# Kernel tuning notes

Measured on AMD Instinct MI355X. Metric: run time of the kernel, lower is better.

The kernel has to match this reference:

```python
import jax, jax.numpy as jnp
import numpy as np

B, S, D, H, DH = 2, 4096, 768, 12, 64
L = 2                      # encoder layers (reduced-depth longformer-base)
HW = 256                   # one-sided sliding window (attention_window = 512)
C = 2 * HW                 # query chunk size
NC = S // C                # number of chunks
KW = C + 2 * HW            # key-window length per chunk
V = 50265
SEP_ID, NSEP = 2, 32       # </s> token id; SEPs per block (fixed by construction)
G = NSEP + 1               # global tokens: <s> at pos 0 + all SEPs
NCLS = 5
EPS = 1e-5
NEG = -1e9


def layer_norm(x, gb):
    m = jnp.mean(x, -1, keepdims=True)
    v = jnp.var(x, -1, keepdims=True)
    return (x - m) * jax.lax.rsqrt(v + EPS) * gb[0] + gb[1]


def split_heads(x):  # [B,S,D] -> [B,H,S,DH]
    return x.reshape(B, S, H, DH).transpose(0, 2, 1, 3)


def window_gather(x):  # [B,H,S,DH] -> [B,H,NC,KW,DH] overlapping key windows
    xp = jnp.pad(x, ((0, 0), (0, 0), (HW, HW), (0, 0)))
    idx = (jnp.arange(NC) * C)[:, None] + jnp.arange(KW)[None, :]
    return xp[:, :, idx, :]


def longformer_attn(x, amask, gpos, wqkv, bqkv, wqkv_g, bqkv_g, wo, bo):
    q = split_heads(x @ wqkv[0] + bqkv[0]) / np.float32(np.sqrt(DH))
    k = split_heads(x @ wqkv[1] + bqkv[1])
    v = split_heads(x @ wqkv[2] + bqkv[2])

    # ----- local sliding-window scores (banded, chunked) -----
    kw = window_gather(k)
    vw = window_gather(v)
    qc = q.reshape(B, H, NC, C, DH)
    s_loc = jnp.einsum('bhncd,bhnkd->bhnck', qc, kw)  # [B,H,NC,C,KW]

    rel = jnp.arange(KW)[None, :] - jnp.arange(C)[:, None]          # [C,KW]
    band_ok = (rel >= 0) & (rel <= 2 * HW)
    key_pos = (jnp.arange(NC) * C)[:, None] + jnp.arange(KW)[None, :] - HW
    in_b = (key_pos >= 0) & (key_pos < S)                            # [NC,KW]
    amp = jnp.pad(amask, ((0, 0), (HW, HW)))
    idx = (jnp.arange(NC) * C)[:, None] + jnp.arange(KW)[None, :]
    am_w = amp[:, idx] > 0                                           # [B,NC,KW]
    mask = band_ok[None, None, None] & in_b[None, None, :, None, :] & am_w[:, None, :, None, :]
    s_loc = jnp.where(mask, s_loc, NEG).reshape(B, H, S, KW)

    # ----- scores of every query against the G global keys -----
    gidx = gpos[:, None, :, None]                                    # [B,1,G,1]
    kg = jnp.take_along_axis(k, gidx, axis=2)                        # [B,H,G,DH]
    vg = jnp.take_along_axis(v, gidx, axis=2)
    s_glob = jnp.einsum('bhsd,bhgd->bhsg', q, kg)                    # [B,H,S,G]

    probs = jax.nn.softmax(jnp.concatenate([s_glob, s_loc], -1), -1)
    pg, pl = probs[..., :G], probs[..., G:]
    ctx = jnp.einsum('bhsg,bhgd->bhsd', pg, vg)
    ctx = ctx + jnp.einsum('bhnck,bhnkd->bhncd', pl.reshape(B, H, NC, C, KW), vw).reshape(B, H, S, DH)

    # ----- global tokens attend to everything (separate projections) -----
    qg = split_heads(x @ wqkv_g[0] + bqkv_g[0]) / np.float32(np.sqrt(DH))
    kgf = split_heads(x @ wqkv_g[1] + bqkv_g[1])
    vgf = split_heads(x @ wqkv_g[2] + bqkv_g[2])
    qg = jnp.take_along_axis(qg, gidx, axis=2)                       # [B,H,G,DH]
    s_g = jnp.einsum('bhgd,bhsd->bhgs', qg, kgf)                     # [B,H,G,S]
    s_g = jnp.where(amask[:, None, None, :] > 0, s_g, NEG)
    og = jnp.einsum('bhgs,bhsd->bhgd', jax.nn.softmax(s_g, -1), vgf)

    ctx_m = ctx.transpose(0, 2, 1, 3).reshape(B, S, D)
    og_m = og.transpose(0, 2, 1, 3).reshape(B, G, D)
    ctx_m = ctx_m.at[jnp.arange(B)[:, None], gpos].set(og_m)         # replace global rows
    return ctx_m @ wo + bo


def setup_inputs() -> dict:
    key = jax.random.key(0)
    ks = jax.random.split(key, 12)
    ids = jax.random.randint(ks[0], (B, S), 5, V, dtype=jnp.int32)
    sep_positions = (jnp.arange(NSEP) + 1) * (S // NSEP) - 1         # SEP every 128 toks
    ids = ids.at[:, sep_positions].set(SEP_ID).at[:, 0].set(0)       # <s> at pos 0
    att = jnp.ones((B, S), jnp.int32)

    def nrm(k, shp):
        return jax.random.normal(k, shp, jnp.float32) * 0.02

    ln = jnp.stack([jnp.ones(D, jnp.float32), jnp.zeros(D, jnp.float32)])
    return dict(
        input_ids=ids, attention_mask=att,
        word_emb=nrm(ks[1], (V, D)), pos_emb=nrm(ks[2], (S + 2, D)),
        type_emb=nrm(ks[3], (D,)), emb_ln=ln,
        Wqkv=nrm(ks[4], (L, 3, D, D)), bqkv=jnp.zeros((L, 3, D), jnp.float32),
        Wqkv_g=nrm(ks[5], (L, 3, D, D)), bqkv_g=jnp.zeros((L, 3, D), jnp.float32),
        Wo=nrm(ks[6], (L, D, D)), bo=jnp.zeros((L, D), jnp.float32),
        ln1=jnp.broadcast_to(ln, (L, 2, D)),
        Wff1=nrm(ks[7], (L, D, 4 * D)), bff1=jnp.zeros((L, 4 * D), jnp.float32),
        Wff2=nrm(ks[8], (L, 4 * D, D)), bff2=jnp.zeros((L, D), jnp.float32),
        ln2=jnp.broadcast_to(ln, (L, 2, D)),
        cls_W=nrm(ks[9], (NCLS, D)), cls_b=jnp.zeros((NCLS,), jnp.float32),
    )


def reference(input_ids, attention_mask, word_emb, pos_emb, type_emb, emb_ln,
              Wqkv, bqkv, Wqkv_g, bqkv_g, Wo, bo, ln1, Wff1, bff1, Wff2, bff2,
              ln2, cls_W, cls_b):
    # global attention mask: pos 0 + every SEP (fixed count by construction)
    sep_pos = jnp.sort(jnp.where(input_ids == SEP_ID, jnp.arange(S)[None, :], S), -1)[:, :NSEP]
    sep_pos = sep_pos.astype(jnp.int32)
    gpos = jnp.concatenate([jnp.zeros((B, 1), jnp.int32), sep_pos], 1)  # [B,G]

    x = word_emb[input_ids] + pos_emb[jnp.arange(S) + 2][None] + type_emb
    x = layer_norm(x, emb_ln)
    for l in range(L):
        a = longformer_attn(x, attention_mask, gpos, Wqkv[l], bqkv[l],
                            Wqkv_g[l], bqkv_g[l], Wo[l], bo[l])
        x = layer_norm(x + a, ln1[l])
        f = jax.nn.gelu(x @ Wff1[l] + bff1[l], approximate=False) @ Wff2[l] + bff2[l]
        x = layer_norm(x + f, ln2[l])

    # gather SEP embeddings (row-major over batch then sentence) -> classifier
    h = jnp.take_along_axis(x, sep_pos[:, :, None], axis=1).reshape(B * NSEP, D)
    return h @ cls_W.T + cls_b
```

## Files before the change

kernel.cpp:

```cpp
#include <hip/hip_runtime.h>


#define Bb 2
#define Ss 4096
#define Dd 768
#define Hh 12
#define Gg 33
#define NSEPn 32
#define Ll 2
#define SPAD 4640
#define PADL 256
#define NCLSn 5
#define NCH 16
#define PARTF 1056
#define PSTR 72

typedef unsigned short u16;
typedef __attribute__((ext_vector_type(8))) short bv8;
typedef __attribute__((ext_vector_type(4))) short sv4;
typedef __attribute__((ext_vector_type(4))) float f32x4;

__device__ __forceinline__ float bf2f(u16 u) {
  unsigned v = ((unsigned)u) << 16;
  return __builtin_bit_cast(float, v);
}
__device__ __forceinline__ u16 f2bf(float f) {
  unsigned u = __builtin_bit_cast(unsigned, f);
  u += 0x7fffu + ((u >> 16) & 1u);
  return (u16)(u >> 16);
}
__device__ __forceinline__ void glds16(const void* g, void* l) {
  __builtin_amdgcn_global_load_lds(
      (const __attribute__((address_space(1))) void*)g,
      (__attribute__((address_space(3))) void*)l, 16, 0, 0);
}

__global__ void sep_find_kernel(const int* __restrict__ ids, int* __restrict__ cnt,
                                int* __restrict__ list) {
  int i = blockIdx.x * 256 + threadIdx.x;
  if (i >= Bb * Ss) return;
  int b = i >> 12;
  if (ids[i] == 2) {
    int idx = atomicAdd(&cnt[b], 1);
    if (idx < 64) list[b * 64 + idx] = i & (Ss - 1);
  }
}

__global__ void sep_sort_kernel(const int* __restrict__ cnt, const int* __restrict__ list,
                                int* __restrict__ gpos) {
  int b = blockIdx.x;
  int t = threadIdx.x;
  int n = cnt[b]; if (n > 64) n = 64;
  if (t < Gg) gpos[b * Gg + t] = (t == 0) ? 0 : (Ss - 1);
  __syncthreads();
  if (t < n) {
    int v = list[b * 64 + t];
    int rank = 0;
    for (int j = 0; j < n; ++j) rank += (list[b * 64 + j] < v) ? 1 : 0;
    if (rank < NSEPn) gpos[b * Gg + 1 + rank] = v;
  }
}

__global__ __launch_bounds__(256)
void wconv_kernel(const float* __restrict__ src0, u16* __restrict__ dst0,
                  int K, int N, int grp, int sstr, long unit, long WLs) {
  __shared__ float t[32][33];
  int z = blockIdx.z;
  const float* src = src0 + (size_t)((z / grp) * sstr + (z % grp)) * K * N;
  u16* dst = dst0 + (size_t)(z / grp) * WLs + (size_t)(z % grp) * unit;
  int n0 = blockIdx.x * 32, k0 = blockIdx.y * 32;
  int tx = threadIdx.x & 31, ty = threadIdx.x >> 5;
  #pragma unroll
  for (int i = 0; i < 4; ++i)
    t[ty + i * 8][tx] = src[(size_t)(k0 + ty + i * 8) * N + n0 + tx];
  __syncthreads();
  #pragma unroll
  for (int i = 0; i < 4; ++i)
    dst[(size_t)(n0 + ty + i * 8) * K + k0 + tx] = f2bf(t[tx][ty + i * 8]);
}

__global__ __launch_bounds__(256)
void embed_ln_kernel(const int* __restrict__ ids, const float* __restrict__ we,
                     const float* __restrict__ pe, const float* __restrict__ te,
                     const float* __restrict__ lnp, float* __restrict__ x,
                     u16* __restrict__ xb) {
  int row = blockIdx.x;
  int s = row & (Ss - 1);
  int id = ids[row];
  int tid = threadIdx.x;
  float v[3]; float sm = 0.f, s2 = 0.f;
  #pragma unroll
  for (int i = 0; i < 3; ++i) {
    int c = tid + i * 256;
    float t = we[(size_t)id * Dd + c] + pe[(size_t)(s + 2) * Dd + c] + te[c];
    v[i] = t; sm += t; s2 += t * t;
  }
  __shared__ float r1[256], r2[256];
  r1[tid] = sm; r2[tid] = s2; __syncthreads();
  for (int o = 128; o; o >>= 1) {
    if (tid < o) { r1[tid] += r1[tid + o]; r2[tid] += r2[tid + o]; }
    __syncthreads();
  }
  float mean = r1[0] * (1.f / 768.f);
  float var  = r2[0] * (1.f / 768.f) - mean * mean;
  float rs = rsqrtf(var + 1e-5f);
  #pragma unroll
  for (int i = 0; i < 3; ++i) {
    int c = tid + i * 256;
    float o = (v[i] - mean) * rs * lnp[c] + lnp[Dd + c];
    x[(size_t)row * Dd + c] = o;
    xb[(size_t)row * Dd + c] = f2bf(o);
  }
}

__global__ __launch_bounds__(256)
void add_ln3_kernel(const float* __restrict__ xin, const float* __restrict__ y0,
                    const u16* __restrict__ y1, const float* __restrict__ lnp,
                    float* __restrict__ xout, u16* __restrict__ xbout) {
  int row = blockIdx.x;
  int tid = threadIdx.x;
  float v[3]; float sm = 0.f, s2 = 0.f;
  #pragma unroll
  for (int i = 0; i < 3; ++i) {
    int c = tid + i * 256;
    size_t idx = (size_t)row * Dd + c;
    float t = xin[idx] + y0[idx] + bf2f(y1[idx]);
    v[i] = t; sm += t; s2 += t * t;
  }
  __shared__ float r1[256], r2[256];
  r1[tid] = sm; r2[tid] = s2; __syncthreads();
  for (int o = 128; o; o >>= 1) {
    if (tid < o) { r1[tid] += r1[tid + o]; r2[tid] += r2[tid + o]; }
    __syncthreads();
  }
  float mean = r1[0] * (1.f / 768.f);
  float var  = r2[0] * (1.f / 768.f) - mean * mean;
  float rs = rsqrtf(var + 1e-5f);
  #pragma unroll
  for (int i = 0; i < 3; ++i) {
    int c = tid + i * 256;
    float o = (v[i] - mean) * rs * lnp[c] + lnp[Dd + c];
    xout[(size_t)row * Dd + c] = o;
    xbout[(size_t)row * Dd + c] = f2bf(o);
  }
}

template <int MODE, bool XSWZ>
__global__ __launch_bounds__(256)
void gemm2_kernel(const u16* __restrict__ A, const u16* __restrict__ Bt,
                  const float* __restrict__ bias, float* __restrict__ outf,
                  u16* __restrict__ o0, u16* __restrict__ o1, u16* __restrict__ o2,
                  u16* __restrict__ o3, u16* __restrict__ o4,
                  int N, int Ks, int Kl, float scale) {
  __shared__ u16 la[2][128 * 32], lb[2][128 * 32];
  int tid = threadIdx.x;
  int wave = tid >> 6, lane = tid & 63;
  int wr = wave >> 1, wc = wave & 1;
  int lg = lane >> 4, lc = lane & 15;
  int bx = blockIdx.x, by = blockIdx.y;
  if (XSWZ) {
    int gx = gridDim.x;
    int nlin = bx + gx * by;
    int NB = gx * gridDim.y;
    nlin = (nlin & 7) * (NB >> 3) + (nlin >> 3);
    bx = nlin % gx;
    by = nlin / gx;
  }
  int row0 = by * 128, col0 = bx * 128;
  int koff = blockIdx.z * Kl;

  int sgr = (lane & 3) ^ ((lane >> 3) & 3);
  const u16* Ag = A + (size_t)(row0 + wave * 32 + (lane >> 2)) * Ks + sgr * 8 + koff;
  const u16* Bg = Bt + (size_t)(col0 + wave * 32 + (lane >> 2)) * Ks + sgr * 8 + koff;
  int wofs = wave * 1024;
  int gph = (lg ^ ((lc >> 1) & 3)) * 8;

  f32x4 acc[4][4];
  #pragma unroll
  for (int m = 0; m < 4; ++m)
    #pragma unroll
    for (int n = 0; n < 4; ++n) acc[m][n] = (f32x4){0.f, 0.f, 0.f, 0.f};

  glds16(Ag, la[0] + wofs);
  glds16(Ag + (size_t)16 * Ks, la[0] + wofs + 512);
  glds16(Bg, lb[0] + wofs);
  glds16(Bg + (size_t)16 * Ks, lb[0] + wofs + 512);
  __syncthreads();

  int nk = Kl >> 5;
  for (int t = 0; t < nk; ++t) {
    int cur = t & 1;
    if (t + 1 < nk) {
      int k1 = (t + 1) << 5;
      glds16(Ag + k1, la[cur ^ 1] + wofs);
      glds16(Ag + (size_t)16 * Ks + k1, la[cur ^ 1] + wofs + 512);
      glds16(Bg + k1, lb[cur ^ 1] + wofs);
      glds16(Bg + (size_t)16 * Ks + k1, lb[cur ^ 1] + wofs + 512);
    }
    bv8 af[4], bf_[4];
    #pragma unroll
    for (int m = 0; m < 4; ++m)
      af[m] = *reinterpret_cast<const bv8*>(la[cur] + (wr * 64 + m * 16 + lc) * 32 + gph);
    #pragma unroll
    for (int n = 0; n < 4; ++n)
      bf_[n] = *reinterpret_cast<const bv8*>(lb[cur] + (wc * 64 + n * 16 + lc) * 32 + gph);
    __builtin_amdgcn_s_setprio(1);
    #pragma unroll
    for (int m = 0; m < 4; ++m)
      #pragma unroll
      for (int n = 0; n < 4; ++n)
        acc[m][n] = __builtin_amdgcn_mfma_f32_16x16x32_bf16(af[m], bf_[n], acc[m][n], 0, 0, 0);
    __builtin_amdgcn_s_setprio(0);
    __syncthreads();
  }

  #pragma unroll
  for (int m = 0; m < 4; ++m) {
    int grow0 = row0 + wr * 64 + m * 16 + lg * 4;
    #pragma unroll
    for (int n = 0; n < 4; ++n) {
      int gcol = col0 + wc * 64 + n * 16 + lc;
      float bvl = bias[gcol];
      if (MODE == 0) {
        if (blockIdx.z == 0) {
          #pragma unroll
          for (int r = 0; r < 4; ++r)
            outf[(size_t)(grow0 + r) * N + gcol] = acc[m][n][r] + bvl;
        } else {
          #pragma unroll
          for (int r = 0; r < 4; ++r)
            o0[(size_t)(grow0 + r) * N + gcol] = f2bf(acc[m][n][r]);
        }
      } else if (MODE == 1) {
        #pragma unroll
        for (int r = 0; r < 4; ++r) {
          float v = acc[m][n][r] + bvl;
          v = 0.5f * v * (1.0f + erff(v * 0.70710678118654752f));
          o0[(size_t)(grow0 + r) * N + gcol] = f2bf(v);
        }
      } else if (MODE == 4) {
        #pragma unroll
        for (int r = 0; r < 4; ++r)
          o0[(size_t)(grow0 + r) * N + gcol] = f2bf((acc[m][n][r] + bvl) * scale);
      } else if (MODE == 2) {
        int sec = (col0 >> 7) / 6;
        int colr = gcol - sec * 768;
        int hh = colr >> 6, d = colr & 63;
        int bb = grow0 >> 12, s = grow0 & (Ss - 1);
        size_t bhh = (size_t)(bb * Hh + hh);
        if (sec == 0) {
          #pragma unroll
          for (int r = 0; r < 4; ++r)
            o0[(bhh * Ss + s + r) * 64 + d] = f2bf((acc[m][n][r] + bvl) * scale);
        } else if (sec == 1) {
          #pragma unroll
          for (int r = 0; r < 4; ++r)
            o1[(bhh * SPAD + PADL + s + r) * 64 + d] = f2bf(acc[m][n][r] + bvl);
        } else if (sec == 2) {
          sv4 pk;
          #pragma unroll
          for (int r = 0; r < 4; ++r) pk[r] = (short)f2bf(acc[m][n][r] + bvl);
          *reinterpret_cast<sv4*>(o2 + (bhh * 64 + d) * SPAD + PADL + s) = pk;
        } else if (sec == 3) {
          #pragma unroll
          for (int r = 0; r < 4; ++r)
            o3[(bhh * Ss + s + r) * 64 + d] = f2bf(acc[m][n][r] + bvl);
        } else {
          sv4 pk;
          #pragma unroll
          for (int r = 0; r < 4; ++r) pk[r] = (short)f2bf(acc[m][n][r] + bvl);
          *reinterpret_cast<sv4*>(o4 + (bhh * 64 + d) * Ss + s) = pk;
        }
      }
    }
  }
}

__global__ __launch_bounds__(256)
void gather_glob_kernel(const u16* __restrict__ kpk, const u16* __restrict__ vtpk,
                        const int* __restrict__ gpos, u16* __restrict__ kg,
                        u16* __restrict__ vgt) {
  int bh = blockIdx.x;
  int b = bh / Hh;
  int tid = threadIdx.x;
  for (int idx = tid; idx < 64 * 64; idx += 256) {
    int g = idx >> 6, d = idx & 63;
    u16 kv = 0, vv = 0;
    if (g < Gg) {
      int p = gpos[b * Gg + g];
      kv = kpk[((size_t)bh * SPAD + PADL + p) * 64 + d];
      vv = vtpk[((size_t)bh * 64 + d) * SPAD + PADL + p];
    }
    kg[(size_t)bh * 4096 + idx] = kv;
    vgt[((size_t)bh * 64 + d) * 64 + g] = vv;
  }
}

__global__ __launch_bounds__(256)
void gather_xg_kernel(const u16* __restrict__ xb, const int* __restrict__ gpos,
                      u16* __restrict__ xg) {
  int rg = blockIdx.x;
  int b = rg / Gg;
  int p = gpos[rg];
  int tid = threadIdx.x;
  for (int c = tid; c < Dd; c += 256)
    xg[(size_t)rg * Dd + c] = xb[((size_t)b * Ss + p) * Dd + c];
}

#define LOCAL_NB (Bb * Hh * (Ss / 64))
__global__ __launch_bounds__(256)
void attn_local_kernel(const u16* __restrict__ qpk, const u16* __restrict__ kpk,
                       const u16* __restrict__ vtpk, const u16* __restrict__ kg,
                       const u16* __restrict__ vgt, const int* __restrict__ amask,
                       u16* __restrict__ ctx) {
  __shared__ u16 Plds[4][16 * PSTR];
  int bid = blockIdx.x;
  int swz = (bid & 7) * (LOCAL_NB / 8) + (bid >> 3);
  int qb = swz & 63;
  int bh = swz >> 6;
  int b = bh / Hh;
  int h = bh - b * Hh;
  int wv = threadIdx.x >> 6;
  int q0 = qb * 64 + wv * 16;
  int lane = threadIdx.x & 63;
  int lg = lane >> 4, lc = lane & 15;
  int lg4 = lg * 4;
  int q = q0 + lc;

  const u16* qbase = qpk + (((size_t)bh) * Ss + q0) * 64;
  bv8 aq0 = *reinterpret_cast<const bv8*>(qbase + (size_t)lc * 64 + lg * 8);
  bv8 aq1 = *reinterpret_cast<const bv8*>(qbase + (size_t)lc * 64 + 32 + lg * 8);

  f32x4 o[4];
  #pragma unroll
  for (int i = 0; i < 4; ++i) o[i] = (f32x4){0.f, 0.f, 0.f, 0.f};
  float mrun = -1e30f, lrun = 0.f;

  const u16* kgb = kg + ((size_t)bh) * 64 * 64;
  const u16* vgb = vgt + ((size_t)bh) * 64 * 64;
  const u16* kb = kpk + ((size_t)bh) * SPAD * 64;
  const u16* vb = vtpk + ((size_t)bh) * 64 * SPAD;
  const int* amb = amask + b * Ss;
  u16* P = &Plds[wv][0];

  bv8 kc[8];
  #pragma unroll
  for (int j = 0; j < 4; ++j) {
    const u16* kr = kgb + (size_t)(j * 16 + lc) * 64;
    kc[2 * j]     = *reinterpret_cast<const bv8*>(kr + lg * 8);
    kc[2 * j + 1] = *reinterpret_cast<const bv8*>(kr + 32 + lg * 8);
  }
  int amvN;
  { int ni = min(max(q0 - 256 + lane, 0), Ss - 1); amvN = amb[ni]; }

  for (int step = 0; step < 10; ++step) {
    bool isg = (step == 0);
    int ks = isg ? 0 : (q0 - 256 + (step - 1) * 64);
    int amvC = amvN;
    if (step < 9) { int ni = min(max(q0 - 256 + step * 64 + lane, 0), Ss - 1); amvN = amb[ni]; }

    bv8 vf0[4];
    #pragma unroll
    for (int nt = 0; nt < 4; ++nt) {
      const u16* vr = isg ? (vgb + (size_t)(nt * 16 + lc) * 64)
                          : (vb + (size_t)(nt * 16 + lc) * SPAD + PADL + ks);
      vf0[nt] = *reinterpret_cast<const bv8*>(vr + lg * 8);
    }
    unsigned long long kmask;
    if (isg) {
      kmask = (1ull << Gg) - 1;
    } else {
      int kidx = ks + lane;
      kmask = __ballot((kidx >= 0) && (kidx < Ss) && (amvC > 0));
    }
    f32x4 sc[4];
    __builtin_amdgcn_s_setprio(1);
    #pragma unroll
    for (int j = 0; j < 4; ++j) {
      f32x4 z = (f32x4){0.f, 0.f, 0.f, 0.f};
      sc[j] = __builtin_amdgcn_mfma_f32_16x16x32_bf16(kc[2 * j], aq0, z, 0, 0, 0);
      sc[j] = __builtin_amdgcn_mfma_f32_16x16x32_bf16(kc[2 * j + 1], aq1, sc[j], 0, 0, 0);
    }
    __builtin_amdgcn_s_setprio(0);
    bv8 vf1[4];
    #pragma unroll
    for (int nt = 0; nt < 4; ++nt) {
      const u16* vr = isg ? (vgb + (size_t)(nt * 16 + lc) * 64 + 32)
                          : (vb + (size_t)(nt * 16 + lc) * SPAD + PADL + ks + 32);
      vf1[nt] = *reinterpret_cast<const bv8*>(vr + lg * 8);
    }
    if (step < 9) {
      int ksn = q0 - 256 + step * 64;
      #pragma unroll
      for (int j = 0; j < 4; ++j) {
        const u16* kr = kb + (size_t)(PADL + ksn + j * 16 + lc) * 64;
        kc[2 * j]     = *reinterpret_cast<const bv8*>(kr + lg * 8);
        kc[2 * j + 1] = *reinterpret_cast<const bv8*>(kr + 32 + lg * 8);
      }
    }
    float mloc = -1e30f;
    bool fast = (!isg) && (step >= 2) && (step <= 8) && (kmask == ~0ull);
    if (fast) {
      #pragma unroll
      for (int j = 0; j < 4; ++j)
        #pragma unroll
        for (int r = 0; r < 4; ++r) mloc = fmaxf(mloc, sc[j][r]);
    } else {
      #pragma unroll
      for (int j = 0; j < 4; ++j)
        #pragma unroll
        for (int r = 0; r < 4; ++r) {
          int kk = ks + j * 16 + lg4 + r;
          bool ok = (kmask >> (j * 16 + lg4 + r)) & 1;
          if (!isg) ok = ok && ((unsigned)(kk - q + 256) <= 512u);
          sc[j][r] = ok ? sc[j][r] : -1e9f;
          mloc = fmaxf(mloc, sc[j][r]);
        }
    }
    mloc = fmaxf(mloc, __shfl_xor(mloc, 16));
    mloc = fmaxf(mloc, __shfl_xor(mloc, 32));
    if (__any(mloc > mrun)) {
      float nm = fmaxf(mrun, mloc);
      float scal = __expf(mrun - nm);
      mrun = nm;
      lrun *= scal;
      #pragma unroll
      for (int r = 0; r < 4; ++r) {
        float sr = __shfl(scal, lg4 + r);
        #pragma unroll
        for (int nt = 0; nt < 4; ++nt) o[nt][r] *= sr;
      }
    }
    float psum = 0.f;
    #pragma unroll
    for (int j = 0; j < 4; ++j) {
      sv4 pk;
      #pragma unroll
      for (int r = 0; r < 4; ++r) {
        float p = __expf(sc[j][r] - mrun);
        psum += p;
        pk[r] = (short)f2bf(p);
      }
      *reinterpret_cast<sv4*>(P + lc * PSTR + j * 16 + lg4) = pk;
    }
    psum += __shfl_xor(psum, 16);
    psum += __shfl_xor(psum, 32);
    lrun += psum;
    __builtin_amdgcn_s_setprio(1);
    {
      bv8 ap = *reinterpret_cast<const bv8*>(P + lc * PSTR + lg * 8);
      #pragma unroll
      for (int nt = 0; nt < 4; ++nt)
        o[nt] = __builtin_amdgcn_mfma_f32_16x16x32_bf16(ap, vf0[nt], o[nt], 0, 0, 0);
      ap = *reinterpret_cast<const bv8*>(P + lc * PSTR + 32 + lg * 8);
      #pragma unroll
      for (int nt = 0; nt < 4; ++nt)
        o[nt] = __builtin_amdgcn_mfma_f32_16x16x32_bf16(ap, vf1[nt], o[nt], 0, 0, 0);
    }
    __builtin_amdgcn_s_setprio(0);
  }
  float inv = 1.0f / lrun;
  #pragma unroll
  for (int r = 0; r < 4; ++r) {
    float invr = __shfl(inv, lg4 + r);
    size_t rowoff = ((size_t)b * Ss + q0 + lg4 + r) * Dd + h * 64;
    #pragma unroll
    for (int nt = 0; nt < 4; ++nt)
      ctx[rowoff + nt * 16 + lc] = f2bf(o[nt][r] * invr);
  }
}

__global__ __launch_bounds__(192)
void attn_globalq_kernel(const u16* __restrict__ qgb, const u16* __restrict__ kgf,
                         const u16* __restrict__ vgt, const int* __restrict__ amask,
                         float* __restrict__ part) {
  __shared__ u16 Plds[3][16 * PSTR];
  int blk = blockIdx.x;
  int ch = blk & (NCH - 1);
  int bh = blk / NCH;
  int b = bh / Hh, h = bh - b * Hh;
  int wv = threadIdx.x >> 6;
  int lane = threadIdx.x & 63;
  int lg = lane >> 4, lc = lane & 15;
  int lg4 = lg * 4;

  int qrow = wv * 16 + lc;
  bv8 aq0 = (bv8)0, aq1 = (bv8)0;
  if (qrow < Gg) {
    const u16* qr = qgb + (size_t)(b * Gg + qrow) * Dd + h * 64;
    aq0 = *reinterpret_cast<const bv8*>(qr + lg * 8);
    aq1 = *reinterpret_cast<const bv8*>(qr + 32 + lg * 8);
  }

  f32x4 o[4];
  #pragma unroll
  for (int i = 0; i < 4; ++i) o[i] = (f32x4){0.f, 0.f, 0.f, 0.f};
  float mrun = -1e30f, lrun = 0.f;

  const u16* kb = kgf + ((size_t)bh) * Ss * 64;
  const u16* vb = vgt + ((size_t)bh) * 64 * Ss;
  const int* amb = amask + b * Ss;
  int ks0 = ch * (Ss / NCH);
  u16* P = &Plds[wv][0];

  bv8 kc[8];
  #pragma unroll
  for (int j = 0; j < 4; ++j) {
    const u16* kr = kb + (size_t)(ks0 + j * 16 + lc) * 64;
    kc[2 * j]     = *reinterpret_cast<const bv8*>(kr + lg * 8);
    kc[2 * j + 1] = *reinterpret_cast<const bv8*>(kr + 32 + lg * 8);
  }

  for (int st = 0; st < 4; ++st) {
    int ks = ks0 + st * 64;
    bv8 vf0[4], vf1[4];
    #pragma unroll
    for (int nt = 0; nt < 4; ++nt) {
      const u16* vr = vb + (size_t)(nt * 16 + lc) * Ss + ks;
      vf0[nt] = *reinterpret_cast<const bv8*>(vr + lg * 8);
      vf1[nt] = *reinterpret_cast<const bv8*>(vr + 32 + lg * 8);
    }
    unsigned long long kmask = __ballot(amb[ks + lane] > 0);
    f32x4 sc[4];
    __builtin_amdgcn_s_setprio(1);
    #pragma unroll
    for (int j = 0; j < 4; ++j) {
      f32x4 z = (f32x4){0.f, 0.f, 0.f, 0.f};
      sc[j] = __builtin_amdgcn_mfma_f32_16x16x32_bf16(kc[2 * j], aq0, z, 0, 0, 0);
      sc[j] = __builtin_amdgcn_mfma_f32_16x16x32_bf16(kc[2 * j + 1], aq1, sc[j], 0, 0, 0);
    }
    __builtin_amdgcn_s_setprio(0);
    if (st < 3) {
      int ksn = ks0 + (st + 1) * 64;
      #pragma unroll
      for (int j = 0; j < 4; ++j) {
        const u16* kr = kb + (size_t)(ksn + j * 16 + lc) * 64;
        kc[2 * j]     = *reinterpret_cast<const bv8*>(kr + lg * 8);
        kc[2 * j + 1] = *reinterpret_cast<const bv8*>(kr + 32 + lg * 8);
      }
    }
    float mloc = -1e30f;
    if (kmask == ~0ull) {
      #pragma unroll
      for (int j = 0; j < 4; ++j)
        #pragma unroll
        for (int r = 0; r < 4; ++r) mloc = fmaxf(mloc, sc[j][r]);
    } else {
      #pragma unroll
      for (int j = 0; j < 4; ++j)
        #pragma unroll
        for (int r = 0; r < 4; ++r) {
          bool ok = (kmask >> (j * 16 + lg4 + r)) & 1;
          sc[j][r] = ok ? sc[j][r] : -1e9f;
          mloc = fmaxf(mloc, sc[j][r]);
        }
    }
    mloc = fmaxf(mloc, __shfl_xor(mloc, 16));
    mloc = fmaxf(mloc, __shfl_xor(mloc, 32));
    if (__any(mloc > mrun)) {
      float nm = fmaxf(mrun, mloc);
      float scal = __expf(mrun - nm);
      mrun = nm;
      lrun *= scal;
      #pragma unroll
      for (int r = 0; r < 4; ++r) {
        float sr = __shfl(scal, lg4 + r);
        #pragma unroll
        for (int nt = 0; nt < 4; ++nt) o[nt][r] *= sr;
      }
    }
    float psum = 0.f;
    #pragma unroll
    for (int j = 0; j < 4; ++j) {
      sv4 pk;
      #pragma unroll
      for (int r = 0; r < 4; ++r) {
        float p = __expf(sc[j][r] - mrun);
        psum += p;
        pk[r] = (short)f2bf(p);
      }
      *reinterpret_cast<sv4*>(P + lc * PSTR + j * 16 + lg4) = pk;
    }
    psum += __shfl_xor(psum, 16);
    psum += __shfl_xor(psum, 32);
    lrun += psum;
    __builtin_amdgcn_s_setprio(1);
    {
      bv8 ap = *reinterpret_cast<const bv8*>(P + lc * PSTR + lg * 8);
      #pragma unroll
      for (int nt = 0; nt < 4; ++nt)
        o[nt] = __builtin_amdgcn_mfma_f32_16x16x32_bf16(ap, vf0[nt], o[nt], 0, 0, 0);
      ap = *reinterpret_cast<const bv8*>(P + lc * PSTR + 32 + lg * 8);
      #pragma unroll
      for (int nt = 0; nt < 4; ++nt)
        o[nt] = __builtin_amdgcn_mfma_f32_16x16x32_bf16(ap, vf1[nt], o[nt], 0, 0, 0);
    }
    __builtin_amdgcn_s_setprio(0);
  }

  float* pb = part + ((size_t)(bh * 3 + wv) * NCH + ch) * PARTF;
  #pragma unroll
  for (int r = 0; r < 4; ++r) {
    int row = lg4 + r;
    #pragma unroll
    for (int nt = 0; nt < 4; ++nt)
      pb[row * 64 + nt * 16 + lc] = o[nt][r];
  }
  if (lg == 0) {
    pb[1024 + lc] = mrun;
    pb[1040 + lc] = lrun;
  }
}

__global__ __launch_bounds__(256)
void attn_gmerge_kernel(const float* __restrict__ part, const int* __restrict__ gpos,
                        u16* __restrict__ ctx) {
  __shared__ float wgt[Gg][NCH];
  __shared__ float sinvl[Gg];
  int bh = blockIdx.x;
  int b = bh / Hh, h = bh - b * Hh;
  int tid = threadIdx.x;
  if (tid < Gg) {
    int qt = tid >> 4, rr = tid & 15;
    const float* pb = part + ((size_t)(bh * 3 + qt) * NCH) * PARTF;
    float mx = -1e30f;
    for (int c = 0; c < NCH; ++c) mx = fmaxf(mx, pb[c * PARTF + 1024 + rr]);
    float l = 0.f;
    for (int c = 0; c < NCH; ++c) {
      float w = __expf(pb[c * PARTF + 1024 + rr] - mx);
      wgt[tid][c] = w;
      l += w * pb[c * PARTF + 1040 + rr];
    }
    sinvl[tid] = 1.0f / l;
  }
  __syncthreads();
  for (int e = tid; e < Gg * 64; e += 256) {
    int row = e >> 6, d = e & 63;
    int qt = row >> 4, rr = row & 15;
    const float* pb = part + ((size_t)(bh * 3 + qt) * NCH) * PARTF + rr * 64 + d;
    float acc = 0.f;
    #pragma unroll
    for (int c = 0; c < NCH; ++c) acc += wgt[row][c] * pb[c * PARTF];
    int pos = gpos[b * Gg + row];
    ctx[((size_t)b * Ss + pos) * Dd + h * 64 + d] = f2bf(acc * sinvl[row]);
  }
}

__global__ __launch_bounds__(64)
void cls_kernel(const float* __restrict__ x, const float* __restrict__ W,
                const float* __restrict__ bias, const int* __restrict__ gpos,
                float* __restrict__ out) {
  int r = blockIdx.x;
  int b = r >> 5, i = r & 31;
  int pos = gpos[b * Gg + 1 + i];
  int lane = threadIdx.x;
  const float* xr = x + ((size_t)b * Ss + pos) * Dd;
  float acc[NCLSn] = {0.f, 0.f, 0.f, 0.f, 0.f};
  for (int k = lane; k < Dd; k += 64) {
    float xv = xr[k];
    #pragma unroll
    for (int c = 0; c < NCLSn; ++c) acc[c] += xv * W[c * Dd + k];
  }
  #pragma unroll
  for (int c = 0; c < NCLSn; ++c) {
    #pragma unroll
    for (int off = 1; off < 64; off <<= 1) acc[c] += __shfl_xor(acc[c], off);
  }
  if (lane == 0) {
    #pragma unroll
    for (int c = 0; c < NCLSn; ++c) out[r * NCLSn + c] = acc[c] + bias[c];
  }
}

extern "C" void kernel_launch(void* const* d_in, const int* in_sizes, int n_in,
                              void* d_out, int out_size, void* d_ws, size_t ws_size,
                              hipStream_t stream) {
  const int* ids     = (const int*)d_in[0];
  const int* amask   = (const int*)d_in[1];
  const float* we    = (const float*)d_in[2];
  const float* pe    = (const float*)d_in[3];
  const float* te    = (const float*)d_in[4];
  const float* embln = (const float*)d_in[5];
  const float* Wqkv  = (const float*)d_in[6];
  const float* bqkv  = (const float*)d_in[7];
  const float* Wqkvg = (const float*)d_in[8];
  const float* bqkvg = (const float*)d_in[9];
  const float* Wo    = (const float*)d_in[10];
  const float* bo    = (const float*)d_in[11];
  const float* ln1   = (const float*)d_in[12];
  const float* Wff1  = (const float*)d_in[13];
  const float* bff1  = (const float*)d_in[14];
  const float* Wff2  = (const float*)d_in[15];
  const float* bff2  = (const float*)d_in[16];
  const float* ln2   = (const float*)d_in[17];
  const float* clsW  = (const float*)d_in[18];
  const float* clsb  = (const float*)d_in[19];
  float* out = (float*)d_out;

  char* ws = (char*)d_ws;
  size_t off = 0;
  auto alloc = [&](size_t bytes) { size_t o = off; off += (bytes + 255) & ~(size_t)255; return o; };

  const size_t DD = (size_t)Dd * Dd;
  const size_t DF = (size_t)Dd * 4 * Dd;
  const size_t WL = 7 * DD + 2 * DF;

  size_t o_cnt  = alloc(Bb * 4);
  size_t o_list = alloc(Bb * 64 * 4);
  size_t o_gpos = alloc(Bb * Gg * 4);
  size_t o_bias = alloc((size_t)Ll * 3840 * 4);
  size_t o_w    = alloc(WL * Ll * 2);
  size_t o_x    = alloc((size_t)Bb * Ss * Dd * 4);
  size_t o_xb   = alloc((size_t)Bb * Ss * Dd * 2);
  size_t o_kgf  = alloc((size_t)Bb * Hh * Ss * 64 * 2);
  size_t o_vgf  = alloc((size_t)Bb * Hh * Ss * 64 * 2);
  size_t o_accB = o_kgf;
  size_t o_qpk  = alloc((size_t)Bb * Hh * Ss * 64 * 2);
  size_t o_kpk  = alloc((size_t)Bb * Hh * SPAD * 64 * 2);
  size_t o_vtpk = alloc((size_t)Bb * Hh * 64 * SPAD * 2);
  size_t o_kg   = alloc((size_t)Bb * Hh * 64 * 64 * 2);
  size_t o_vgt  = alloc((size_t)Bb * Hh * 64 * 64 * 2);
  size_t o_xg   = alloc((size_t)128 * Dd * 2);
  size_t o_qg   = alloc((size_t)128 * Dd * 2);
  size_t o_part = alloc((size_t)Bb * Hh * 3 * NCH * PARTF * 4);
  size_t o_f1b  = o_qpk;
  {
    size_t f1b_bytes = (size_t)Bb * Ss * 4 * Dd * 2;
    if (off - o_qpk < f1b_bytes) off = o_qpk + ((f1b_bytes + 255) & ~(size_t)255);
  }
  size_t o_ctx = alloc((size_t)Bb * Ss * Dd * 2);
  size_t o_acc = alloc((size_t)Bb * Ss * Dd * 4);
  if (ws_size < off) return;

  u16* Wb = (u16*)(ws + o_w);
  int* gposp = (int*)(ws + o_gpos);
  float* accA = (float*)(ws + o_acc);
  u16* accB = (u16*)(ws + o_accB);

  (void)hipMemsetAsync(ws + o_cnt, 0, Bb * 4, stream);
  (void)hipMemsetAsync(ws + o_kpk, 0, (size_t)Bb * Hh * SPAD * 64 * 2, stream);
  (void)hipMemsetAsync(ws + o_vtpk, 0, (size_t)Bb * Hh * 64 * SPAD * 2, stream);
  (void)hipMemsetAsync(ws + o_xg, 0, (size_t)128 * Dd * 2, stream);

  for (int l = 0; l < Ll; ++l) {
    (void)hipMemcpyAsync(ws + o_bias + (size_t)l * 3840 * 4, bqkv + (size_t)l * 3 * Dd,
                         3 * Dd * 4, hipMemcpyDeviceToDevice, stream);
    (void)hipMemcpyAsync(ws + o_bias + (size_t)l * 3840 * 4 + 3 * Dd * 4,
                         bqkvg + (size_t)(l * 3 + 1) * Dd,
                         2 * Dd * 4, hipMemcpyDeviceToDevice, stream);
  }

  sep_find_kernel<<<(Bb * Ss + 255) / 256, 256, 0, stream>>>(ids, (int*)(ws + o_cnt), (int*)(ws + o_list));
  sep_sort_kernel<<<Bb, 64, 0, stream>>>((int*)(ws + o_cnt), (int*)(ws + o_list), gposp);

  wconv_kernel<<<dim3(24, 24, 6), 256, 0, stream>>>(Wqkv,       Wb,          Dd, Dd, 3, 3, (long)DD, (long)WL);
  wconv_kernel<<<dim3(24, 24, 2), 256, 0, stream>>>(Wqkvg + DD,     Wb + 3 * DD, Dd, Dd, 1, 3, 0L, (long)WL);
  wconv_kernel<<<dim3(24, 24, 2), 256, 0, stream>>>(Wqkvg + 2 * DD, Wb + 4 * DD, Dd, Dd, 1, 3, 0L, (long)WL);
  wconv_kernel<<<dim3(24, 24, 2), 256, 0, stream>>>(Wqkvg,          Wb + 5 * DD, Dd, Dd, 1, 3, 0L, (long)WL);
  wconv_kernel<<<dim3(24, 24, 2), 256, 0, stream>>>(Wo,         Wb + 6 * DD, Dd, Dd, 1, 1, 0L, (long)WL);
  wconv_kernel<<<dim3(96, 24, 2), 256, 0, stream>>>(Wff1,       Wb + 7 * DD, Dd, 4 * Dd, 1, 1, 0L, (long)WL);
  wconv_kernel<<<dim3(24, 96, 2), 256, 0, stream>>>(Wff2,       Wb + 7 * DD + DF, 4 * Dd, Dd, 1, 1, 0L, (long)WL);

  embed_ln_kernel<<<Bb * Ss, 256, 0, stream>>>(ids, we, pe, te, embln, (float*)(ws + o_x), (u16*)(ws + o_xb));

  for (int l = 0; l < Ll; ++l) {
    size_t wb = (size_t)l * WL;
    u16* xb = (u16*)(ws + o_xb);
    gemm2_kernel<2, true><<<dim3(30, 64), 256, 0, stream>>>(xb, Wb + wb, (float*)(ws + o_bias) + (size_t)l * 3840,
        nullptr,
        (u16*)(ws + o_qpk), (u16*)(ws + o_kpk), (u16*)(ws + o_vtpk),
        (u16*)(ws + o_kgf), (u16*)(ws + o_vgf), 3840, Dd, Dd, 0.125f);
    gather_glob_kernel<<<Bb * Hh, 256, 0, stream>>>((u16*)(ws + o_kpk), (u16*)(ws + o_vtpk), gposp, (u16*)(ws + o_kg), (u16*)(ws + o_vgt));
    gather_xg_kernel<<<Bb * Gg, 256, 0, stream>>>(xb, gposp, (u16*)(ws + o_xg));
    gemm2_kernel<4, false><<<dim3(6, 1), 256, 0, stream>>>((u16*)(ws + o_xg), Wb + wb + 5 * DD, bqkvg + (size_t)l * 3 * Dd,
        nullptr, (u16*)(ws + o_qg), nullptr, nullptr, nullptr, nullptr, Dd, Dd, Dd, 0.125f);
    attn_local_kernel<<<LOCAL_NB, 256, 0, stream>>>((u16*)(ws + o_qpk), (u16*)(ws + o_kpk), (u16*)(ws + o_vtpk), (u16*)(ws + o_kg), (u16*)(ws + o_vgt), amask, (u16*)(ws + o_ctx));
    attn_globalq_kernel<<<Bb * Hh * NCH, 192, 0, stream>>>((u16*)(ws + o_qg), (u16*)(ws + o_kgf), (u16*)(ws + o_vgf), amask, (float*)(ws + o_part));
    attn_gmerge_kernel<<<Bb * Hh, 256, 0, stream>>>((float*)(ws + o_part), gposp, (u16*)(ws + o_ctx));
    gemm2_kernel<0, true><<<dim3(6, 64, 2), 256, 0, stream>>>((u16*)(ws + o_ctx), Wb + wb + 6 * DD, bo + (size_t)l * Dd, accA,
        accB, nullptr, nullptr, nullptr, nullptr, Dd, Dd, Dd / 2, 1.0f);
    add_ln3_kernel<<<Bb * Ss, 256, 0, stream>>>((float*)(ws + o_x), accA, accB, ln1 + (size_t)l * 2 * Dd, (float*)(ws + o_x), xb);
    gemm2_kernel<1, true><<<dim3(24, 64), 256, 0, stream>>>(xb, Wb + wb + 7 * DD, bff1 + (size_t)l * 4 * Dd, nullptr,
        (u16*)(ws + o_f1b), nullptr, nullptr, nullptr, nullptr, 4 * Dd, Dd, Dd, 1.0f);
    gemm2_kernel<0, true><<<dim3(6, 64, 2), 256, 0, stream>>>((u16*)(ws + o_f1b), Wb + wb + 7 * DD + DF, bff2 + (size_t)l * Dd, accA,
        accB, nullptr, nullptr, nullptr, nullptr, Dd, 4 * Dd, 2 * Dd, 1.0f);
    add_ln3_kernel<<<Bb * Ss, 256, 0, stream>>>((float*)(ws + o_x), accA, accB, ln2 + (size_t)l * 2 * Dd, (float*)(ws + o_x), xb);
  }

  cls_kernel<<<Bb * NSEPn, 64, 0, stream>>>((float*)(ws + o_x), clsW, clsb, gposp, out);
}
```

Measured before the change: 840.4 us.

## Process two query tiles per wave in local attention and defer softmax rescaling

The local sliding-window attention kernel now runs 2 waves per block, and each wave handles 32 queries as two 16-row tiles. The key and value fragments loaded for a step feed MFMAs for both tiles, which halves global K/V fragment traffic per query and interleaves independent MFMA chains. Online-softmax rescaling of the accumulators is now skipped unless the new maximum exceeds the running one by more than 8, in both the local and the global-query kernels. The cost is higher register pressure per wave and fewer waves per block, which may lower occupancy or latency hiding.

```diff
diff --git a/kernel.cpp b/kernel.cpp
--- a/kernel.cpp
+++ b/kernel.cpp
@@ -308,7 +308,7 @@
 }
 
 #define LOCAL_NB (Bb * Hh * (Ss / 64))
-__global__ __launch_bounds__(256)
+__global__ __launch_bounds__(128)
 void attn_local_kernel(const u16* __restrict__ qpk, const u16* __restrict__ kpk,
                        const u16* __restrict__ vtpk, const u16* __restrict__ kg,
                        const u16* __restrict__ vgt, const int* __restrict__ amask,
@@ -321,27 +321,32 @@
   int b = bh / Hh;
   int h = bh - b * Hh;
   int wv = threadIdx.x >> 6;
-  int q0 = qb * 64 + wv * 16;
+  int q0 = qb * 64;
+  int qA = q0 + wv * 32;
   int lane = threadIdx.x & 63;
   int lg = lane >> 4, lc = lane & 15;
   int lg4 = lg * 4;
-  int q = q0 + lc;
-
-  const u16* qbase = qpk + (((size_t)bh) * Ss + q0) * 64;
-  bv8 aq0 = *reinterpret_cast<const bv8*>(qbase + (size_t)lc * 64 + lg * 8);
-  bv8 aq1 = *reinterpret_cast<const bv8*>(qbase + (size_t)lc * 64 + 32 + lg * 8);
-
-  f32x4 o[4];
-  #pragma unroll
-  for (int i = 0; i < 4; ++i) o[i] = (f32x4){0.f, 0.f, 0.f, 0.f};
-  float mrun = -1e30f, lrun = 0.f;
+  int qa = qA + lc, qbq = qA + 16 + lc;
+
+  const u16* qrowA = qpk + ((size_t)bh * Ss + qA + lc) * 64;
+  bv8 aqA0 = *reinterpret_cast<const bv8*>(qrowA + lg * 8);
+  bv8 aqA1 = *reinterpret_cast<const bv8*>(qrowA + 32 + lg * 8);
+  const u16* qrowB = qrowA + 16 * 64;
+  bv8 aqB0 = *reinterpret_cast<const bv8*>(qrowB + lg * 8);
+  bv8 aqB1 = *reinterpret_cast<const bv8*>(qrowB + 32 + lg * 8);
+
+  f32x4 oA[4], oB[4];
+  #pragma unroll
+  for (int i = 0; i < 4; ++i) { oA[i] = (f32x4){0.f,0.f,0.f,0.f}; oB[i] = (f32x4){0.f,0.f,0.f,0.f}; }
+  float mrunA = -1e30f, lrunA = 0.f, mrunB = -1e30f, lrunB = 0.f;
 
   const u16* kgb = kg + ((size_t)bh) * 64 * 64;
   const u16* vgb = vgt + ((size_t)bh) * 64 * 64;
   const u16* kb = kpk + ((size_t)bh) * SPAD * 64;
   const u16* vb = vtpk + ((size_t)bh) * 64 * SPAD;
   const int* amb = amask + b * Ss;
-  u16* P = &Plds[wv][0];
+  u16* PA = &Plds[wv * 2][0];
+  u16* PB = &Plds[wv * 2 + 1][0];
 
   bv8 kc[8];
   #pragma unroll
@@ -359,12 +364,13 @@
     int amvC = amvN;
     if (step < 9) { int ni = min(max(q0 - 256 + step * 64 + lane, 0), Ss - 1); amvN = amb[ni]; }
 
-    bv8 vf0[4];
+    bv8 vf0[4], vf1[4];
     #pragma unroll
     for (int nt = 0; nt < 4; ++nt) {
       const u16* vr = isg ? (vgb + (size_t)(nt * 16 + lc) * 64)
                           : (vb + (size_t)(nt * 16 + lc) * SPAD + PADL + ks);
       vf0[nt] = *reinterpret_cast<const bv8*>(vr + lg * 8);
+      vf1[nt] = *reinterpret_cast<const bv8*>(vr + 32 + lg * 8);
     }
     unsigned long long kmask;
     if (isg) {
@@ -373,22 +379,17 @@
       int kidx = ks + lane;
       kmask = __ballot((kidx >= 0) && (kidx < Ss) && (amvC > 0));
     }
-    f32x4 sc[4];
+    f32x4 scA[4], scB[4];
     __builtin_amdgcn_s_setprio(1);
     #pragma unroll
     for (int j = 0; j < 4; ++j) {
       f32x4 z = (f32x4){0.f, 0.f, 0.f, 0.f};
-      sc[j] = __builtin_amdgcn_mfma_f32_16x16x32_bf16(kc[2 * j], aq0, z, 0, 0, 0);
-      sc[j] = __builtin_amdgcn_mfma_f32_16x16x32_bf16(kc[2 * j + 1], aq1, sc[j], 0, 0, 0);
+      scA[j] = __builtin_amdgcn_mfma_f32_16x16x32_bf16(kc[2 * j], aqA0, z, 0, 0, 0);
+      scA[j] = __builtin_amdgcn_mfma_f32_16x16x32_bf16(kc[2 * j + 1], aqA1, scA[j], 0, 0, 0);
+      scB[j] = __builtin_amdgcn_mfma_f32_16x16x32_bf16(kc[2 * j], aqB0, z, 0, 0, 0);
+      scB[j] = __builtin_amdgcn_mfma_f32_16x16x32_bf16(kc[2 * j + 1], aqB1, scB[j], 0, 0, 0);
     }
     __builtin_amdgcn_s_setprio(0);
-    bv8 vf1[4];
-    #pragma unroll
-    for (int nt = 0; nt < 4; ++nt) {
-      const u16* vr = isg ? (vgb + (size_t)(nt * 16 + lc) * 64 + 32)
-                          : (vb + (size_t)(nt * 16 + lc) * SPAD + PADL + ks + 32);
-      vf1[nt] = *reinterpret_cast<const bv8*>(vr + lg * 8);
-    }
     if (step < 9) {
       int ksn = q0 - 256 + step * 64;
       #pragma unroll
@@ -398,75 +399,114 @@
         kc[2 * j + 1] = *reinterpret_cast<const bv8*>(kr + 32 + lg * 8);
       }
     }
-    float mloc = -1e30f;
     bool fast = (!isg) && (step >= 2) && (step <= 8) && (kmask == ~0ull);
+    float mlocA = -1e30f, mlocB = -1e30f;
     if (fast) {
       #pragma unroll
       for (int j = 0; j < 4; ++j)
         #pragma unroll
-        for (int r = 0; r < 4; ++r) mloc = fmaxf(mloc, sc[j][r]);
+        for (int r = 0; r < 4; ++r) {
+          mlocA = fmaxf(mlocA, scA[j][r]);
+          mlocB = fmaxf(mlocB, scB[j][r]);
+        }
     } else {
       #pragma unroll
       for (int j = 0; j < 4; ++j)
         #pragma unroll
         for (int r = 0; r < 4; ++r) {
           int kk = ks + j * 16 + lg4 + r;
-          bool ok = (kmask >> (j * 16 + lg4 + r)) & 1;
-          if (!isg) ok = ok && ((unsigned)(kk - q + 256) <= 512u);
-          sc[j][r] = ok ? sc[j][r] : -1e9f;
-          mloc = fmaxf(mloc, sc[j][r]);
+          bool okk = (kmask >> (j * 16 + lg4 + r)) & 1;
+          bool okA = okk, okB = okk;
+          if (!isg) {
+            okA = okA && ((unsigned)(kk - qa + 256) <= 512u);
+            okB = okB && ((unsigned)(kk - qbq + 256) <= 512u);
+          }
+          scA[j][r] = okA ? scA[j][r] : -1e9f;
+          scB[j][r] = okB ? scB[j][r] : -1e9f;
+          mlocA = fmaxf(mlocA, scA[j][r]);
+          mlocB = fmaxf(mlocB, scB[j][r]);
         }
     }
-    mloc = fmaxf(mloc, __shfl_xor(mloc, 16));
-    mloc = fmaxf(mloc, __shfl_xor(mloc, 32));
-    if (__any(mloc > mrun)) {
-      float nm = fmaxf(mrun, mloc);
-      float scal = __expf(mrun - nm);
-      mrun = nm;
-      lrun *= scal;
+    mlocA = fmaxf(mlocA, __shfl_xor(mlocA, 16));
+    mlocA = fmaxf(mlocA, __shfl_xor(mlocA, 32));
+    mlocB = fmaxf(mlocB, __shfl_xor(mlocB, 16));
+    mlocB = fmaxf(mlocB, __shfl_xor(mlocB, 32));
+    if (__any(mlocA > mrunA + 8.f)) {
+      float nm = fmaxf(mrunA, mlocA);
+      float scal = __expf(mrunA - nm);
+      mrunA = nm;
+      lrunA *= scal;
       #pragma unroll
       for (int r = 0; r < 4; ++r) {
         float sr = __shfl(scal, lg4 + r);
         #pragma unroll
-        for (int nt = 0; nt < 4; ++nt) o[nt][r] *= sr;
-      }
-    }
-    float psum = 0.f;
+        for (int nt = 0; nt < 4; ++nt) oA[nt][r] *= sr;
+      }
+    }
+    if (__any(mlocB > mrunB + 8.f)) {
+      float nm = fmaxf(mrunB, mlocB);
+      float scal = __expf(mrunB - nm);
+      mrunB = nm;
+      lrunB *= scal;
+      #pragma unroll
+      for (int r = 0; r < 4; ++r) {
+        float sr = __shfl(scal, lg4 + r);
+        #pragma unroll
+        for (int nt = 0; nt < 4; ++nt) oB[nt][r] *= sr;
+      }
+    }
+    float psumA = 0.f, psumB = 0.f;
     #pragma unroll
     for (int j = 0; j < 4; ++j) {
-      sv4 pk;
+      sv4 pkA, pkB;
       #pragma unroll
       for (int r = 0; r < 4; ++r) {
-        float p = __expf(sc[j][r] - mrun);
-        psum += p;
-        pk[r] = (short)f2bf(p);
-      }
-      *reinterpret_cast<sv4*>(P + lc * PSTR + j * 16 + lg4) = pk;
-    }
-    psum += __shfl_xor(psum, 16);
-    psum += __shfl_xor(psum, 32);
-    lrun += psum;
+        float pA = __expf(scA[j][r] - mrunA);
+        float pB = __expf(scB[j][r] - mrunB);
+        psumA += pA; psumB += pB;
+        pkA[r] = (short)f2bf(pA);
+        pkB[r] = (short)f2bf(pB);
+      }
+      *reinterpret_cast<sv4*>(PA + lc * PSTR + j * 16 + lg4) = pkA;
+      *reinterpret_cast<sv4*>(PB + lc * PSTR + j * 16 + lg4) = pkB;
+    }
+    psumA += __shfl_xor(psumA, 16);
+    psumA += __shfl_xor(psumA, 32);
+    psumB += __shfl_xor(psumB, 16);
+    psumB += __shfl_xor(psumB, 32);
+    lrunA += psumA;
+    lrunB += psumB;
     __builtin_amdgcn_s_setprio(1);
     {
-      bv8 ap = *reinterpret_cast<const bv8*>(P + lc * PSTR + lg * 8);
-      #pragma unroll
-      for (int nt = 0; nt < 4; ++nt)
-        o[nt] = __builtin_amdgcn_mfma_f32_16x16x32_bf16(ap, vf0[nt], o[nt], 0, 0, 0);
-      ap = *reinterpret_cast<const bv8*>(P + lc * PSTR + 32 + lg * 8);
-      #pragma unroll
-      for (int nt = 0; nt < 4; ++nt)
-        o[nt] = __builtin_amdgcn_mfma_f32_16x16x32_bf16(ap, vf1[nt], o[nt], 0, 0, 0);
+      bv8 apA = *reinterpret_cast<const bv8*>(PA + lc * PSTR + lg * 8);
+      bv8 apB = *reinterpret_cast<const bv8*>(PB + lc * PSTR + lg * 8);
+      #pragma unroll
+      for (int nt = 0; nt < 4; ++nt) {
+        oA[nt] = __builtin_amdgcn_mfma_f32_16x16x32_bf16(apA, vf0[nt], oA[nt], 0, 0, 0);
+        oB[nt] = __builtin_amdgcn_mfma_f32_16x16x32_bf16(apB, vf0[nt], oB[nt], 0, 0, 0);
+      }
+      apA = *reinterpret_cast<const bv8*>(PA + lc * PSTR + 32 + lg * 8);
+      apB = *reinterpret_cast<const bv8*>(PB + lc * PSTR + 32 + lg * 8);
+      #pragma unroll
+      for (int nt = 0; nt < 4; ++nt) {
+        oA[nt] = __builtin_amdgcn_mfma_f32_16x16x32_bf16(apA, vf1[nt], oA[nt], 0, 0, 0);
+        oB[nt] = __builtin_amdgcn_mfma_f32_16x16x32_bf16(apB, vf1[nt], oB[nt], 0, 0, 0);
+      }
     }
     __builtin_amdgcn_s_setprio(0);
   }
-  float inv = 1.0f / lrun;
+  float invA = 1.0f / lrunA, invB = 1.0f / lrunB;
   #pragma unroll
   for (int r = 0; r < 4; ++r) {
-    float invr = __shfl(inv, lg4 + r);
-    size_t rowoff = ((size_t)b * Ss + q0 + lg4 + r) * Dd + h * 64;
-    #pragma unroll
-    for (int nt = 0; nt < 4; ++nt)
-      ctx[rowoff + nt * 16 + lc] = f2bf(o[nt][r] * invr);
+    float invrA = __shfl(invA, lg4 + r);
+    float invrB = __shfl(invB, lg4 + r);
+    size_t rowA = ((size_t)b * Ss + qA + lg4 + r) * Dd + h * 64;
+    size_t rowB = rowA + (size_t)16 * Dd;
+    #pragma unroll
+    for (int nt = 0; nt < 4; ++nt) {
+      ctx[rowA + nt * 16 + lc] = f2bf(oA[nt][r] * invrA);
+      ctx[rowB + nt * 16 + lc] = f2bf(oB[nt][r] * invrB);
+    }
   }
 }
 
@@ -557,7 +597,7 @@
     }
     mloc = fmaxf(mloc, __shfl_xor(mloc, 16));
     mloc = fmaxf(mloc, __shfl_xor(mloc, 32));
-    if (__any(mloc > mrun)) {
+    if (__any(mloc > mrun + 8.f)) {
       float nm = fmaxf(mrun, mloc);
       float scal = __expf(mrun - nm);
       mrun = nm;
@@ -774,7 +814,7 @@
     gather_xg_kernel<<<Bb * Gg, 256, 0, stream>>>(xb, gposp, (u16*)(ws + o_xg));
     gemm2_kernel<4, false><<<dim3(6, 1), 256, 0, stream>>>((u16*)(ws + o_xg), Wb + wb + 5 * DD, bqkvg + (size_t)l * 3 * Dd,
         nullptr, (u16*)(ws + o_qg), nullptr, nullptr, nullptr, nullptr, Dd, Dd, Dd, 0.125f);
-    attn_local_kernel<<<LOCAL_NB, 256, 0, stream>>>((u16*)(ws + o_qpk), (u16*)(ws + o_kpk), (u16*)(ws + o_vtpk), (u16*)(ws + o_kg), (u16*)(ws + o_vgt), amask, (u16*)(ws + o_ctx));
+    attn_local_kernel<<<LOCAL_NB, 128, 0, stream>>>((u16*)(ws + o_qpk), (u16*)(ws + o_kpk), (u16*)(ws + o_vtpk), (u16*)(ws + o_kg), (u16*)(ws + o_vgt), amask, (u16*)(ws + o_ctx));
     attn_globalq_kernel<<<Bb * Hh * NCH, 192, 0, stream>>>((u16*)(ws + o_qg), (u16*)(ws + o_kgf), (u16*)(ws + o_vgf), amask, (float*)(ws + o_part));
     attn_gmerge_kernel<<<Bb * Hh, 256, 0, stream>>>((float*)(ws + o_part), gposp, (u16*)(ws + o_ctx));
     gemm2_kernel<0, true><<<dim3(6, 64, 2), 256, 0, stream>>>((u16*)(ws + o_ctx), Wb + wb + 6 * DD, bo + (size_t)l * Dd, accA,
```

Result: faster. 776.8 us (-7.6%).
